# Optimization experiments

Measured on AMD Instinct MI355X. Metric: run time of the kernel, lower is better.

Reference implementation:

```python
import jax, jax.numpy as jnp
import numpy as np

N = 40000        # total gene nodes
E = 640000       # edges
F_IN = 128       # num_features
H = 128          # hidden_dim
SUB = 400        # genes per cell
EPS = 1e-5


def _bn(x, g, b):
    # BatchNorm1d, training-mode batch statistics (biased variance), deterministic
    m = x.mean(axis=0)
    v = x.var(axis=0)
    return (x - m) * jax.lax.rsqrt(v + EPS) * g + b


def _gcn_conv(x, W, b, src, dst):
    # PyG GCNConv: h = X W; add self-loops; symmetric deg^{-1/2} normalization;
    # scatter-add messages from src into dst; then add bias.
    h = x @ W                                   # [N, H]
    loop = jnp.arange(N)
    s = jnp.concatenate([src, loop])            # [E+N]
    d = jnp.concatenate([dst, loop])
    deg = jax.ops.segment_sum(jnp.ones(s.shape[0], h.dtype), d, num_segments=N)
    dis = jnp.where(deg > 0, deg ** -0.5, 0.0)  # deg_inv_sqrt
    norm = dis[s] * dis[d]                      # [E+N]
    out = jax.ops.segment_sum(h[s] * norm[:, None], d, num_segments=N)
    return out + b


def setup_inputs() -> dict:
    key = jax.random.key(0)
    ks = jax.random.split(key, 16)
    sc = lambda fan: 1.0 / np.sqrt(fan)
    inp = {
        "x": jax.random.normal(ks[0], (N, F_IN), jnp.float32),
        "edge_index": jax.random.randint(ks[1], (2, E), 0, N, jnp.int64),
        "conv1_w": jax.random.normal(ks[2], (F_IN, H), jnp.float32) * sc(F_IN),
        "conv1_b": jnp.zeros((H,), jnp.float32),
        "bn1_g": jnp.ones((H,), jnp.float32),
        "bn1_b": jnp.zeros((H,), jnp.float32),
        "conv2_w": jax.random.normal(ks[3], (H, H), jnp.float32) * sc(H),
        "conv2_b": jnp.zeros((H,), jnp.float32),
        "bn2_g": jnp.ones((H,), jnp.float32),
        "bn2_b": jnp.zeros((H,), jnp.float32),
        "att_w1": jax.random.normal(ks[4], (H, H // 2), jnp.float32) * sc(H),
        "att_b1": jnp.zeros((H // 2,), jnp.float32),
        "att_w2": jax.random.normal(ks[5], (H // 2, 1), jnp.float32) * sc(H // 2),
        "att_b2": jnp.zeros((1,), jnp.float32),
        "fc_w": jax.random.normal(ks[6], (H, H), jnp.float32) * sc(H),
        "fc_b": jnp.zeros((H,), jnp.float32),
        "bne_g": jnp.ones((H,), jnp.float32),
        "bne_b": jnp.zeros((H,), jnp.float32),
        "bot_w": jax.random.normal(ks[7], (H, 32), jnp.float32) * sc(H),
        "bot_b": jnp.zeros((32,), jnp.float32),
        "bnb_g": jnp.ones((32,), jnp.float32),
        "bnb_b": jnp.zeros((32,), jnp.float32),
    }
    return inp


def reference(x, edge_index, conv1_w, conv1_b, bn1_g, bn1_b,
              conv2_w, conv2_b, bn2_g, bn2_b,
              att_w1, att_b1, att_w2, att_b2,
              fc_w, fc_b, bne_g, bne_b,
              bot_w, bot_b, bnb_g, bnb_b):
    src, dst = edge_index[0], edge_index[1]
    # embed: two GCNConv + BN + ReLU (dropout omitted: deterministic reference)
    h = jax.nn.relu(_bn(_gcn_conv(x, conv1_w, conv1_b, src, dst), bn1_g, bn1_b))
    emb = jax.nn.relu(_bn(_gcn_conv(h, conv2_w, conv2_b, src, dst), bn2_g, bn2_b))
    # attention pooling over genes within each cell
    num_cells = N // SUB
    xr = emb.reshape(num_cells, SUB, H)                      # [C, S, H]
    scores = jnp.tanh(xr @ att_w1 + att_b1) @ att_w2 + att_b2  # [C, S, 1]
    w = jax.nn.softmax(scores, axis=1)
    pooled = jnp.sum(xr * w, axis=1)                          # [C, H]
    # dense head
    y = jax.nn.relu(_bn(pooled @ fc_w + fc_b, bne_g, bne_b))
    y = jax.nn.relu(_bn(y @ bot_w + bot_b, bnb_g, bnb_b))     # [C, 32]
    return (y, emb)
```

## Files before the change

kernel.cpp:

```cpp
#include <hip/hip_runtime.h>
#include <math.h>

typedef unsigned int u32;
typedef __attribute__((ext_vector_type(8))) short bf16x8;
typedef __attribute__((ext_vector_type(4))) float f32x4;

#define NN   40000
#define EE   640000
#define SUBG 400
#define CELLS 100
#define BNEPS 1e-5f
#define GB   2048
#define GEMMB 625
#define FILLB 1024

__device__ __forceinline__ u32 bf16pair(float a, float b) {
    u32 ua = __float_as_uint(a), ub = __float_as_uint(b);
    ua += 0x7fffu + ((ua >> 16) & 1u);
    ub += 0x7fffu + ((ub >> 16) & 1u);
    return (ua >> 16) | (ub & 0xffff0000u);
}
__device__ __forceinline__ float bflo(u32 u) { return __uint_as_float(u << 16); }
__device__ __forceinline__ float bfhi(u32 u) { return __uint_as_float(u & 0xffff0000u); }

#define SWZ(g, cc) ( ((cc) & 3) | (((((cc) >> 2) ^ ((g) & 15))) << 2) )

__global__ void k_init(int* deg_cursor, const float* W1, u32* Wt1,
                       const float* W2, u32* Wt2, const float* wa, u32* Wta,
                       float* hstats) {
    int i = blockIdx.x * 256 + threadIdx.x;
    if (i < 2 * NN) { deg_cursor[i] = 0; return; }
    i -= 2 * NN;
    if (i < 16384) {
        const float* W = (i < 8192) ? W1 : W2;
        u32* Wt = (i < 8192) ? Wt1 : Wt2;
        int j = i & 8191;
        int n = j >> 6, k2 = (j & 63) * 2;
        Wt[n * 64 + (j & 63)] = bf16pair(W[k2 * 128 + n], W[(k2 + 1) * 128 + n]);
        return;
    }
    i -= 16384;
    if (i < 4096) {
        int n = i >> 6, k2 = (i & 63) * 2;
        Wta[n * 64 + (i & 63)] = bf16pair(wa[k2 * 64 + n], wa[(k2 + 1) * 64 + n]);
        return;
    }
    i -= 4096;
    if (i < 320) hstats[i] = 0.f;
}

__global__ void k_degcount(const int* __restrict__ dst, int* __restrict__ deg) {
    int i = blockIdx.x * blockDim.x + threadIdx.x;
    int stride = gridDim.x * blockDim.x;
    for (; i < EE; i += stride) atomicAdd(&deg[dst[i]], 1);
}

__global__ __launch_bounds__(1024)
void k_scan(const int* __restrict__ deg, int* __restrict__ rowstart,
            float* __restrict__ dis) {
    __shared__ int ps[1024];
    int t = threadIdx.x;
    const int4* d4 = (const int4*)deg;
    int sum = 0;
#pragma unroll
    for (int j = 0; j < 10; ++j) {
        int i4 = t * 10 + j;
        if (i4 < 10000) {
            int4 v = d4[i4];
            sum += v.x + v.y + v.z + v.w;
        }
    }
    ps[t] = sum;
    __syncthreads();
    for (int off = 1; off < 1024; off <<= 1) {
        int add = (t >= off) ? ps[t - off] : 0;
        __syncthreads();
        ps[t] += add;
        __syncthreads();
    }
    int run = ps[t] - sum;
#pragma unroll
    for (int j = 0; j < 10; ++j) {
        int i4 = t * 10 + j;
        if (i4 < 10000) {
            int4 v = d4[i4];
            int4 r;
            r.x = run;
            r.y = run + v.x;
            r.z = r.y + v.y;
            r.w = r.z + v.z;
            run = r.w + v.w;
            *(int4*)&rowstart[i4 * 4] = r;
            float4 dv;
            dv.x = rsqrtf((float)(v.x + 1));
            dv.y = rsqrtf((float)(v.y + 1));
            dv.z = rsqrtf((float)(v.z + 1));
            dv.w = rsqrtf((float)(v.w + 1));
            *(float4*)&dis[i4 * 4] = dv;
        }
    }
    if (t == 0) rowstart[NN] = EE;
}

__global__ __launch_bounds__(256)
void k_fillgemm(const float* __restrict__ X, const u32* __restrict__ Wt,
                u32* __restrict__ Yb, const float* __restrict__ dis,
                const int* __restrict__ src, const int* __restrict__ dst,
                const int* __restrict__ rowstart, int* __restrict__ cursor,
                int* __restrict__ csr_src) {
    int bid = blockIdx.x;
    int t = threadIdx.x;
    if (bid >= GEMMB) {
        int i = (bid - GEMMB) * 256 + t;
        int stride = FILLB * 256;
        for (; i < EE; i += stride) {
            int d = dst[i];
            int slot = rowstart[d] + atomicAdd(&cursor[d], 1);
            csr_src[slot] = src[i];
        }
        return;
    }
    int l = t & 63, wv = t >> 6;
    int rowbase = bid * 64 + wv * 16;
    int ml = l & 15, kg = l >> 4;

    f32x4 acc[8];
#pragma unroll
    for (int nt = 0; nt < 8; ++nt) acc[nt] = (f32x4){0.f, 0.f, 0.f, 0.f};
    const float* xr = X + (long)(rowbase + ml) * 128;
#pragma unroll
    for (int kk = 0; kk < 4; ++kk) {
        int k0 = kk * 32 + kg * 8;
        float4 xa = *(const float4*)&xr[k0];
        float4 xb = *(const float4*)&xr[k0 + 4];
        union { u32 u[4]; bf16x8 v; } af;
        af.u[0] = bf16pair(xa.x, xa.y);
        af.u[1] = bf16pair(xa.z, xa.w);
        af.u[2] = bf16pair(xb.x, xb.y);
        af.u[3] = bf16pair(xb.z, xb.w);
#pragma unroll
        for (int nt = 0; nt < 8; ++nt) {
            bf16x8 b = *(const bf16x8*)&Wt[(nt * 16 + ml) * 64 + (k0 >> 1)];
            acc[nt] = __builtin_amdgcn_mfma_f32_16x16x32_bf16(af.v, b, acc[nt], 0, 0, 0);
        }
    }
#pragma unroll
    for (int r = 0; r < 4; ++r) {
        int m = rowbase + kg * 4 + r;
        float dd = dis[m];
        long obase = (long)m * 64;
#pragma unroll
        for (int nt = 0; nt < 8; ++nt) {
            float v = acc[nt][r] * dd;
            float v2 = __shfl_xor(v, 1);
            if ((l & 1) == 0)
                Yb[obase + nt * 8 + (ml >> 1)] = bf16pair(v, v2);
        }
    }
}

__global__ __launch_bounds__(256)
void k_gemm_bf16(const u32* __restrict__ Xb, const u32* __restrict__ Wt,
                 u32* __restrict__ Yb, const float* __restrict__ ss,
                 const float* __restrict__ dis) {
    int t = threadIdx.x;
    int l = t & 63, wv = t >> 6;
    int rowbase = blockIdx.x * 64 + wv * 16;
    int ml = l & 15, kg = l >> 4;

    f32x4 acc[8];
#pragma unroll
    for (int nt = 0; nt < 8; ++nt) acc[nt] = (f32x4){0.f, 0.f, 0.f, 0.f};
    const u32* xr = Xb + (long)(rowbase + ml) * 64;
#pragma unroll
    for (int kk = 0; kk < 4; ++kk) {
        int k0 = kk * 32 + kg * 8;
        uint4 xw = *(const uint4*)&xr[k0 >> 1];
        float f0 = bflo(xw.x), f1 = bfhi(xw.x), f2 = bflo(xw.y), f3 = bfhi(xw.y);
        float f4 = bflo(xw.z), f5 = bfhi(xw.z), f6 = bflo(xw.w), f7 = bfhi(xw.w);
        float4 sca = *(const float4*)&ss[k0];
        float4 sha = *(const float4*)&ss[128 + k0];
        float4 scb = *(const float4*)&ss[k0 + 4];
        float4 shb = *(const float4*)&ss[128 + k0 + 4];
        f0 = fmaxf(fmaf(f0, sca.x, sha.x), 0.f);
        f1 = fmaxf(fmaf(f1, sca.y, sha.y), 0.f);
        f2 = fmaxf(fmaf(f2, sca.z, sha.z), 0.f);
        f3 = fmaxf(fmaf(f3, sca.w, sha.w), 0.f);
        f4 = fmaxf(fmaf(f4, scb.x, shb.x), 0.f);
        f5 = fmaxf(fmaf(f5, scb.y, shb.y), 0.f);
        f6 = fmaxf(fmaf(f6, scb.z, shb.z), 0.f);
        f7 = fmaxf(fmaf(f7, scb.w, shb.w), 0.f);
        union { u32 u[4]; bf16x8 v; } af;
        af.u[0] = bf16pair(f0, f1);
        af.u[1] = bf16pair(f2, f3);
        af.u[2] = bf16pair(f4, f5);
        af.u[3] = bf16pair(f6, f7);
#pragma unroll
        for (int nt = 0; nt < 8; ++nt) {
            bf16x8 b = *(const bf16x8*)&Wt[(nt * 16 + ml) * 64 + (k0 >> 1)];
            acc[nt] = __builtin_amdgcn_mfma_f32_16x16x32_bf16(af.v, b, acc[nt], 0, 0, 0);
        }
    }
#pragma unroll
    for (int r = 0; r < 4; ++r) {
        int m = rowbase + kg * 4 + r;
        float dd = dis[m];
        long obase = (long)m * 64;
#pragma unroll
        for (int nt = 0; nt < 8; ++nt) {
            float v = acc[nt][r] * dd;
            float v2 = __shfl_xor(v, 1);
            if ((l & 1) == 0)
                Yb[obase + nt * 8 + (ml >> 1)] = bf16pair(v, v2);
        }
    }
}

__global__ __launch_bounds__(256)
void k_gather_stats(const uint4* __restrict__ Hb, const int* __restrict__ rowstart,
                    const int* __restrict__ csr_src, const float* __restrict__ dis,
                    const float* __restrict__ bias, u32* __restrict__ F1b,
                    float* __restrict__ part) {
    __shared__ float ls[1024], lq[1024];
    int t = threadIdx.x;
    int lane = t & 63, wv = t >> 6;
    int gw = blockIdx.x * 4 + wv;
    int g = lane >> 4, p = lane & 15;
    int c0 = p * 8 + g * 2;
    float2 bb = *(const float2*)&bias[c0];
    float s0 = 0.f, s1 = 0.f, q0 = 0.f, q1 = 0.f;

    for (int node = gw; node < NN; node += GB * 4) {
        float a0 = 0.f, a1 = 0.f, a2 = 0.f, a3 = 0.f, a4 = 0.f, a5 = 0.f, a6 = 0.f, a7 = 0.f;
        if (g == 0) {
            uint4 h = Hb[node * 16 + p];
            a0 = bflo(h.x); a1 = bfhi(h.x);
            a2 = bflo(h.y); a3 = bfhi(h.y);
            a4 = bflo(h.z); a5 = bfhi(h.z);
            a6 = bflo(h.w); a7 = bfhi(h.w);
        }
        int e1 = rowstart[node + 1];
        int e = rowstart[node] + g;
        for (; e + 4 < e1; e += 8) {
            int sA = csr_src[e];
            int sB = csr_src[e + 4];
            uint4 h0 = Hb[sA * 16 + p];
            uint4 h1 = Hb[sB * 16 + p];
            a0 += bflo(h0.x); a1 += bfhi(h0.x);
            a2 += bflo(h0.y); a3 += bfhi(h0.y);
            a4 += bflo(h0.z); a5 += bfhi(h0.z);
            a6 += bflo(h0.w); a7 += bfhi(h0.w);
            a0 += bflo(h1.x); a1 += bfhi(h1.x);
            a2 += bflo(h1.y); a3 += bfhi(h1.y);
            a4 += bflo(h1.z); a5 += bfhi(h1.z);
            a6 += bflo(h1.w); a7 += bfhi(h1.w);
        }
        if (e < e1) {
            int sA = csr_src[e];
            uint4 h0 = Hb[sA * 16 + p];
            a0 += bflo(h0.x); a1 += bfhi(h0.x);
            a2 += bflo(h0.y); a3 += bfhi(h0.y);
            a4 += bflo(h0.z); a5 += bfhi(h0.z);
            a6 += bflo(h0.w); a7 += bfhi(h0.w);
        }
#pragma unroll
        for (int m = 16; m <= 32; m <<= 1) {
            a0 += __shfl_xor(a0, m); a1 += __shfl_xor(a1, m);
            a2 += __shfl_xor(a2, m); a3 += __shfl_xor(a3, m);
            a4 += __shfl_xor(a4, m); a5 += __shfl_xor(a5, m);
            a6 += __shfl_xor(a6, m); a7 += __shfl_xor(a7, m);
        }
        float dd = dis[node];
        float x = (g == 0) ? a0 : (g == 1) ? a2 : (g == 2) ? a4 : a6;
        float y = (g == 0) ? a1 : (g == 1) ? a3 : (g == 2) ? a5 : a7;
        x = fmaf(x, dd, bb.x);
        y = fmaf(y, dd, bb.y);
        u32 pw = bf16pair(x, y);
        F1b[node * 64 + (c0 >> 1)] = pw;
        float rx = bflo(pw), ry = bfhi(pw);
        s0 += rx; s1 += ry; q0 += rx * rx; q1 += ry * ry;
    }
    ls[wv * 128 + c0] = s0; ls[wv * 128 + c0 + 1] = s1;
    lq[wv * 128 + c0] = q0; lq[wv * 128 + c0 + 1] = q1;
    __syncthreads();
    if (t < 128) {
        float S = ls[t] + ls[128 + t] + ls[256 + t] + ls[384 + t];
        float Q = lq[t] + lq[128 + t] + lq[256 + t] + lq[384 + t];
        part[blockIdx.x * 256 + t] = S;
        part[blockIdx.x * 256 + 128 + t] = Q;
    }
}

__global__ __launch_bounds__(256)
void k_bnfinalw(const float* __restrict__ part, const float* __restrict__ g,
                const float* __restrict__ b, float* __restrict__ ss) {
    __shared__ float rs[256], rq[256];
    int c = blockIdx.x, t = threadIdx.x;
    float s = 0.f, q = 0.f;
    for (int i = t; i < GB; i += 256) {
        s += part[i * 256 + c];
        q += part[i * 256 + 128 + c];
    }
    rs[t] = s; rq[t] = q;
    __syncthreads();
    for (int off = 128; off > 0; off >>= 1) {
        if (t < off) { rs[t] += rs[t + off]; rq[t] += rq[t + off]; }
        __syncthreads();
    }
    if (t == 0) {
        float mean = rs[0] * (1.0f / NN);
        float var  = rq[0] * (1.0f / NN) - mean * mean;
        float sc = g[c] * rsqrtf(var + BNEPS);
        ss[c] = sc;
        ss[128 + c] = b[c] - mean * sc;
    }
}

__global__ __launch_bounds__(512, 1)
void k_cell(const u32* __restrict__ F1b, const float* __restrict__ ss,
            float* __restrict__ emb,
            const u32* __restrict__ Wta, const float* __restrict__ b1,
            const float* __restrict__ w2, const float* __restrict__ b2,
            const float* __restrict__ fc_w, const float* __restrict__ fc_b,
            float* __restrict__ y1pre, float* __restrict__ hstats) {
    __shared__ u32 xs[SUBG * 64];
    __shared__ float sc[SUBG];
    __shared__ float red[512];
    __shared__ float pr[128];
    int c = blockIdx.x;
    int t = threadIdx.x;
    long gbase = (long)c * SUBG;

    for (int i = t; i < SUBG * 64; i += 512) {
        int gg = i >> 6, cc = i & 63;
        u32 v = F1b[(gbase + gg) * 64 + cc];
        float x0 = bflo(v), x1 = bfhi(v);
        float2 scv = *(const float2*)&ss[2 * cc];
        float2 shv = *(const float2*)&ss[128 + 2 * cc];
        x0 = fmaxf(fmaf(x0, scv.x, shv.x), 0.f);
        x1 = fmaxf(fmaf(x1, scv.y, shv.y), 0.f);
        float2 o = { x0, x1 };
        *(float2*)&emb[(gbase + gg) * 128 + 2 * cc] = o;
        xs[gg * 64 + SWZ(gg, cc)] = bf16pair(x0, x1);
    }
    __syncthreads();

    int l = t & 63, wv = t >> 6;
    int ml = l & 15, kg = l >> 4;
    bf16x8 bw[4][4];
#pragma unroll
    for (int nt = 0; nt < 4; ++nt)
#pragma unroll
        for (int kk = 0; kk < 4; ++kk)
            bw[nt][kk] = *(const bf16x8*)&Wta[(nt * 16 + ml) * 64 + (kk * 16 + kg * 4)];
    float b1v[4], w2v[4];
#pragma unroll
    for (int nt = 0; nt < 4; ++nt) {
        b1v[nt] = b1[nt * 16 + ml];
        w2v[nt] = w2[nt * 16 + ml];
    }
    float b2v = b2[0];

    for (int tile = wv; tile < 25; tile += 8) {
        int gg = tile * 16 + ml;
        f32x4 acc[4];
#pragma unroll
        for (int nt = 0; nt < 4; ++nt) acc[nt] = (f32x4){0.f, 0.f, 0.f, 0.f};
#pragma unroll
        for (int kk = 0; kk < 4; ++kk) {
            int cc4 = kk * 4 + kg;
            bf16x8 a = *(const bf16x8*)&xs[gg * 64 + ((cc4 ^ ml) << 2)];
#pragma unroll
            for (int nt = 0; nt < 4; ++nt)
                acc[nt] = __builtin_amdgcn_mfma_f32_16x16x32_bf16(a, bw[nt][kk], acc[nt], 0, 0, 0);
        }
#pragma unroll
        for (int r = 0; r < 4; ++r) {
            int g2 = tile * 16 + kg * 4 + r;
            float s = tanhf(acc[0][r] + b1v[0]) * w2v[0]
                    + tanhf(acc[1][r] + b1v[1]) * w2v[1]
                    + tanhf(acc[2][r] + b1v[2]) * w2v[2]
                    + tanhf(acc[3][r] + b1v[3]) * w2v[3];
            s += __shfl_xor(s, 1);
            s += __shfl_xor(s, 2);
            s += __shfl_xor(s, 4);
            s += __shfl_xor(s, 8);
            if (ml == 0) sc[g2] = s + b2v;
        }
    }
    __syncthreads();

    red[t] = (t < SUBG) ? sc[t] : -1e30f;
    __syncthreads();
    for (int off = 256; off > 0; off >>= 1) {
        if (t < off) red[t] = fmaxf(red[t], red[t + off]);
        __syncthreads();
    }
    float mx = red[0];
    __syncthreads();
    float e = 0.f;
    if (t < SUBG) { e = __expf(sc[t] - mx); }
    red[t] = e;
    __syncthreads();
    for (int off = 256; off > 0; off >>= 1) {
        if (t < off) red[t] += red[t + off];
        __syncthreads();
    }
    float inv = 1.0f / red[0];
    __syncthreads();
    if (t < SUBG) sc[t] = e * inv;
    __syncthreads();

    int col = t & 127, grp = t >> 7;
    int cc = col >> 1, lohi = col & 1;
    float acc = 0.f;
    for (int gg = grp; gg < SUBG; gg += 4) {
        u32 v = xs[gg * 64 + SWZ(gg, cc)];
        float val = lohi ? bfhi(v) : bflo(v);
        acc += sc[gg] * val;
    }
    red[t] = acc;
    __syncthreads();
    if (t < 128) pr[col] = red[col] + red[128 + col] + red[256 + col] + red[384 + col];
    __syncthreads();

    if (t < 128) {
        float a1 = fc_b[t];
#pragma unroll 4
        for (int k = 0; k < 128; ++k) a1 = fmaf(pr[k], fc_w[k * 128 + t], a1);
        y1pre[c * 128 + t] = a1;
        atomicAdd(&hstats[t], a1);
        atomicAdd(&hstats[128 + t], a1 * a1);
    }
}

__global__ __launch_bounds__(128)
void k_head2s(const float* __restrict__ y1pre, const float* __restrict__ hstats,
              const float* __restrict__ bne_g, const float* __restrict__ bne_b,
              const float* __restrict__ bot_w, const float* __restrict__ bot_b,
              float* __restrict__ y2pre, float* __restrict__ hstats2) {
    __shared__ float row[128];
    int c = blockIdx.x, t = threadIdx.x;
    float s = hstats[t], q = hstats[128 + t];
    float mean = s * 0.01f, var = q * 0.01f - mean * mean;
    float scv = bne_g[t] * rsqrtf(var + BNEPS);
    float shv = bne_b[t] - mean * scv;
    row[t] = fmaxf(fmaf(y1pre[c * 128 + t], scv, shv), 0.f);
    __syncthreads();
    if (t < 32) {
        float a2 = bot_b[t];
#pragma unroll 4
        for (int k = 0; k < 128; ++k) a2 = fmaf(row[k], bot_w[k * 32 + t], a2);
        y2pre[c * 32 + t] = a2;
        atomicAdd(&hstats2[t], a2);
        atomicAdd(&hstats2[32 + t], a2 * a2);
    }
}

__global__ __launch_bounds__(256)
void k_out(const float* __restrict__ y2pre, const float* __restrict__ hstats2,
           const float* __restrict__ bnb_g, const float* __restrict__ bnb_b,
           float* __restrict__ y_out) {
    __shared__ float scv[32], shv[32];
    int t = threadIdx.x;
    if (t < 32) {
        float s = hstats2[t], q = hstats2[32 + t];
        float mean = s * 0.01f, var = q * 0.01f - mean * mean;
        float v = bnb_g[t] * rsqrtf(var + BNEPS);
        scv[t] = v; shv[t] = bnb_b[t] - mean * v;
    }
    __syncthreads();
    for (int i = t; i < CELLS * 32; i += 256)
        y_out[i] = fmaxf(fmaf(y2pre[i], scv[i & 31], shv[i & 31]), 0.f);
}

extern "C" void kernel_launch(void* const* d_in, const int* in_sizes, int n_in,
                              void* d_out, int out_size, void* d_ws, size_t ws_size,
                              hipStream_t stream) {
    const float* x        = (const float*)d_in[0];
    const int*   ei       = (const int*)d_in[1];
    const float* conv1_w  = (const float*)d_in[2];
    const float* conv1_b  = (const float*)d_in[3];
    const float* bn1_g    = (const float*)d_in[4];
    const float* bn1_b    = (const float*)d_in[5];
    const float* conv2_w  = (const float*)d_in[6];
    const float* conv2_b  = (const float*)d_in[7];
    const float* bn2_g    = (const float*)d_in[8];
    const float* bn2_b    = (const float*)d_in[9];
    const float* att_w1   = (const float*)d_in[10];
    const float* att_b1   = (const float*)d_in[11];
    const float* att_w2   = (const float*)d_in[12];
    const float* att_b2   = (const float*)d_in[13];
    const float* fc_w     = (const float*)d_in[14];
    const float* fc_b     = (const float*)d_in[15];
    const float* bne_g    = (const float*)d_in[16];
    const float* bne_b    = (const float*)d_in[17];
    const float* bot_w    = (const float*)d_in[18];
    const float* bot_b    = (const float*)d_in[19];
    const float* bnb_g    = (const float*)d_in[20];
    const float* bnb_b    = (const float*)d_in[21];

    const int* src = ei;
    const int* dst = ei + EE;

    float* y_out   = (float*)d_out;
    float* emb_out = y_out + CELLS * 32;

    float* ws = (float*)d_ws;
    u32*   Hb     = (u32*)ws;
    u32*   F1b    = Hb + (long)NN * 64;
    float* dis    = (float*)(F1b + (long)NN * 64);
    float* part   = dis + NN;
    float* ss     = part + GB * 256;
    float* hstats = ss + 256;
    float* y1pre  = hstats + 320;
    float* y2pre  = y1pre + CELLS * 128;
    u32*   Wt1    = (u32*)(y2pre + CELLS * 32);
    u32*   Wt2    = Wt1 + 8192;
    u32*   Wta    = Wt2 + 8192;
    int*   deg    = (int*)(Wta + 4096);
    int*   cursor = deg + NN;
    int*   rowstart = cursor + NN;
    int*   csr_src  = rowstart + NN + 1;

    k_init<<<394, 256, 0, stream>>>(deg, conv1_w, Wt1, conv2_w, Wt2, att_w1, Wta, hstats);
    k_degcount<<<512, 256, 0, stream>>>(dst, deg);
    k_scan<<<1, 1024, 0, stream>>>(deg, rowstart, dis);
    k_fillgemm<<<GEMMB + FILLB, 256, 0, stream>>>(x, Wt1, Hb, dis, src, dst,
                                                  rowstart, cursor, csr_src);
    k_gather_stats<<<GB, 256, 0, stream>>>((const uint4*)Hb, rowstart, csr_src, dis,
                                           conv1_b, F1b, part);
    k_bnfinalw<<<128, 256, 0, stream>>>(part, bn1_g, bn1_b, ss);
    k_gemm_bf16<<<GEMMB, 256, 0, stream>>>(F1b, Wt2, Hb, ss, dis);
    k_gather_stats<<<GB, 256, 0, stream>>>((const uint4*)Hb, rowstart, csr_src, dis,
                                           conv2_b, F1b, part);
    k_bnfinalw<<<128, 256, 0, stream>>>(part, bn2_g, bn2_b, ss);
    k_cell<<<CELLS, 512, 0, stream>>>(F1b, ss, emb_out, Wta, att_b1, att_w2, att_b2,
                                      fc_w, fc_b, y1pre, hstats);
    k_head2s<<<CELLS, 128, 0, stream>>>(y1pre, hstats, bne_g, bne_b, bot_w, bot_b,
                                        y2pre, hstats + 256);
    k_out<<<1, 256, 0, stream>>>(y2pre, hstats + 256, bnb_g, bnb_b, y_out);
}
```

Baseline: 244.4 us.

## Split per-cell attention kernel across many blocks and move first GEMM earlier

```diff
diff --git a/kernel.cpp b/kernel.cpp
--- a/kernel.cpp
+++ b/kernel.cpp
@@ -10,9 +10,11 @@
 #define SUBG 400
 #define CELLS 100
 #define BNEPS 1e-5f
-#define GB   2048
+#define GB    2048
 #define GEMMB 625
+#define DEGB  512
 #define FILLB 1024
+#define SCALEB 2500
 
 __device__ __forceinline__ u32 bf16pair(float a, float b) {
     u32 ua = __float_as_uint(a), ub = __float_as_uint(b);
@@ -22,8 +24,6 @@
 }
 __device__ __forceinline__ float bflo(u32 u) { return __uint_as_float(u << 16); }
 __device__ __forceinline__ float bfhi(u32 u) { return __uint_as_float(u & 0xffff0000u); }
-
-#define SWZ(g, cc) ( ((cc) & 3) | (((((cc) >> 2) ^ ((g) & 15))) << 2) )
 
 __global__ void k_init(int* deg_cursor, const float* W1, u32* Wt1,
                        const float* W2, u32* Wt2, const float* wa, u32* Wta,
@@ -49,10 +49,54 @@
     if (i < 320) hstats[i] = 0.f;
 }
 
-__global__ void k_degcount(const int* __restrict__ dst, int* __restrict__ deg) {
-    int i = blockIdx.x * blockDim.x + threadIdx.x;
-    int stride = gridDim.x * blockDim.x;
-    for (; i < EE; i += stride) atomicAdd(&deg[dst[i]], 1);
+__global__ __launch_bounds__(256)
+void k_gemmdeg(const float* __restrict__ X, const u32* __restrict__ Wt,
+               u32* __restrict__ Yb, const int* __restrict__ dst,
+               int* __restrict__ deg) {
+    int bid = blockIdx.x;
+    int t = threadIdx.x;
+    if (bid >= GEMMB) {
+        int i = (bid - GEMMB) * 256 + t;
+        int stride = DEGB * 256;
+        for (; i < EE; i += stride) atomicAdd(&deg[dst[i]], 1);
+        return;
+    }
+    int l = t & 63, wv = t >> 6;
+    int rowbase = bid * 64 + wv * 16;
+    int ml = l & 15, kg = l >> 4;
+
+    f32x4 acc[8];
+#pragma unroll
+    for (int nt = 0; nt < 8; ++nt) acc[nt] = (f32x4){0.f, 0.f, 0.f, 0.f};
+    const float* xr = X + (long)(rowbase + ml) * 128;
+#pragma unroll
+    for (int kk = 0; kk < 4; ++kk) {
+        int k0 = kk * 32 + kg * 8;
+        float4 xa = *(const float4*)&xr[k0];
+        float4 xb = *(const float4*)&xr[k0 + 4];
+        union { u32 u[4]; bf16x8 v; } af;
+        af.u[0] = bf16pair(xa.x, xa.y);
+        af.u[1] = bf16pair(xa.z, xa.w);
+        af.u[2] = bf16pair(xb.x, xb.y);
+        af.u[3] = bf16pair(xb.z, xb.w);
+#pragma unroll
+        for (int nt = 0; nt < 8; ++nt) {
+            bf16x8 b = *(const bf16x8*)&Wt[(nt * 16 + ml) * 64 + (k0 >> 1)];
+            acc[nt] = __builtin_amdgcn_mfma_f32_16x16x32_bf16(af.v, b, acc[nt], 0, 0, 0);
+        }
+    }
+#pragma unroll
+    for (int r = 0; r < 4; ++r) {
+        int m = rowbase + kg * 4 + r;
+        long obase = (long)m * 64;
+#pragma unroll
+        for (int nt = 0; nt < 8; ++nt) {
+            float v = acc[nt][r];
+            float v2 = __shfl_xor(v, 1);
+            if ((l & 1) == 0)
+                Yb[obase + nt * 8 + (ml >> 1)] = bf16pair(v, v2);
+        }
+    }
 }
 
 __global__ __launch_bounds__(1024)
@@ -103,15 +147,14 @@
 }
 
 __global__ __launch_bounds__(256)
-void k_fillgemm(const float* __restrict__ X, const u32* __restrict__ Wt,
-                u32* __restrict__ Yb, const float* __restrict__ dis,
-                const int* __restrict__ src, const int* __restrict__ dst,
-                const int* __restrict__ rowstart, int* __restrict__ cursor,
-                int* __restrict__ csr_src) {
+void k_fillscale(const int* __restrict__ src, const int* __restrict__ dst,
+                 const int* __restrict__ rowstart, int* __restrict__ cursor,
+                 int* __restrict__ csr_src, uint4* __restrict__ Hb,
+                 const float* __restrict__ dis) {
     int bid = blockIdx.x;
     int t = threadIdx.x;
-    if (bid >= GEMMB) {
-        int i = (bid - GEMMB) * 256 + t;
+    if (bid < FILLB) {
+        int i = bid * 256 + t;
         int stride = FILLB * 256;
         for (; i < EE; i += stride) {
             int d = dst[i];
@@ -120,43 +163,14 @@
         }
         return;
     }
-    int l = t & 63, wv = t >> 6;
-    int rowbase = bid * 64 + wv * 16;
-    int ml = l & 15, kg = l >> 4;
-
-    f32x4 acc[8];
-#pragma unroll
-    for (int nt = 0; nt < 8; ++nt) acc[nt] = (f32x4){0.f, 0.f, 0.f, 0.f};
-    const float* xr = X + (long)(rowbase + ml) * 128;
-#pragma unroll
-    for (int kk = 0; kk < 4; ++kk) {
-        int k0 = kk * 32 + kg * 8;
-        float4 xa = *(const float4*)&xr[k0];
-        float4 xb = *(const float4*)&xr[k0 + 4];
-        union { u32 u[4]; bf16x8 v; } af;
-        af.u[0] = bf16pair(xa.x, xa.y);
-        af.u[1] = bf16pair(xa.z, xa.w);
-        af.u[2] = bf16pair(xb.x, xb.y);
-        af.u[3] = bf16pair(xb.z, xb.w);
-#pragma unroll
-        for (int nt = 0; nt < 8; ++nt) {
-            bf16x8 b = *(const bf16x8*)&Wt[(nt * 16 + ml) * 64 + (k0 >> 1)];
-            acc[nt] = __builtin_amdgcn_mfma_f32_16x16x32_bf16(af.v, b, acc[nt], 0, 0, 0);
-        }
-    }
-#pragma unroll
-    for (int r = 0; r < 4; ++r) {
-        int m = rowbase + kg * 4 + r;
-        float dd = dis[m];
-        long obase = (long)m * 64;
-#pragma unroll
-        for (int nt = 0; nt < 8; ++nt) {
-            float v = acc[nt][r] * dd;
-            float v2 = __shfl_xor(v, 1);
-            if ((l & 1) == 0)
-                Yb[obase + nt * 8 + (ml >> 1)] = bf16pair(v, v2);
-        }
-    }
+    int i = (bid - FILLB) * 256 + t;
+    float dd = dis[i >> 4];
+    uint4 v = Hb[i];
+    v.x = bf16pair(bflo(v.x) * dd, bfhi(v.x) * dd);
+    v.y = bf16pair(bflo(v.y) * dd, bfhi(v.y) * dd);
+    v.z = bf16pair(bflo(v.z) * dd, bfhi(v.z) * dd);
+    v.w = bf16pair(bflo(v.w) * dd, bfhi(v.w) * dd);
+    Hb[i] = v;
 }
 
 __global__ __launch_bounds__(256)
@@ -316,43 +330,55 @@
     }
 }
 
-__global__ __launch_bounds__(512, 1)
-void k_cell(const u32* __restrict__ F1b, const float* __restrict__ ss,
-            float* __restrict__ emb,
-            const u32* __restrict__ Wta, const float* __restrict__ b1,
-            const float* __restrict__ w2, const float* __restrict__ b2,
-            const float* __restrict__ fc_w, const float* __restrict__ fc_b,
-            float* __restrict__ y1pre, float* __restrict__ hstats) {
-    __shared__ u32 xs[SUBG * 64];
-    __shared__ float sc[SUBG];
-    __shared__ float red[512];
-    __shared__ float pr[128];
-    int c = blockIdx.x;
-    int t = threadIdx.x;
-    long gbase = (long)c * SUBG;
-
-    for (int i = t; i < SUBG * 64; i += 512) {
-        int gg = i >> 6, cc = i & 63;
-        u32 v = F1b[(gbase + gg) * 64 + cc];
-        float x0 = bflo(v), x1 = bfhi(v);
-        float2 scv = *(const float2*)&ss[2 * cc];
-        float2 shv = *(const float2*)&ss[128 + 2 * cc];
-        x0 = fmaxf(fmaf(x0, scv.x, shv.x), 0.f);
-        x1 = fmaxf(fmaf(x1, scv.y, shv.y), 0.f);
-        float2 o = { x0, x1 };
-        *(float2*)&emb[(gbase + gg) * 128 + 2 * cc] = o;
-        xs[gg * 64 + SWZ(gg, cc)] = bf16pair(x0, x1);
-    }
-    __syncthreads();
-
+__global__ __launch_bounds__(256)
+void k_scoremb(const u32* __restrict__ F1b, const float* __restrict__ ss,
+               float* __restrict__ emb,
+               const u32* __restrict__ Wta, const float* __restrict__ b1,
+               const float* __restrict__ w2, const float* __restrict__ b2,
+               float* __restrict__ scores) {
+    int t = threadIdx.x;
     int l = t & 63, wv = t >> 6;
+    int rowbase = blockIdx.x * 64 + wv * 16;
     int ml = l & 15, kg = l >> 4;
-    bf16x8 bw[4][4];
-#pragma unroll
-    for (int nt = 0; nt < 4; ++nt)
-#pragma unroll
-        for (int kk = 0; kk < 4; ++kk)
-            bw[nt][kk] = *(const bf16x8*)&Wta[(nt * 16 + ml) * 64 + (kk * 16 + kg * 4)];
+
+    f32x4 acc[4];
+#pragma unroll
+    for (int nt = 0; nt < 4; ++nt) acc[nt] = (f32x4){0.f, 0.f, 0.f, 0.f};
+    const u32* xr = F1b + (long)(rowbase + ml) * 64;
+    float* er = emb + (long)(rowbase + ml) * 128;
+#pragma unroll
+    for (int kk = 0; kk < 4; ++kk) {
+        int k0 = kk * 32 + kg * 8;
+        uint4 xw = *(const uint4*)&xr[k0 >> 1];
+        float f0 = bflo(xw.x), f1 = bfhi(xw.x), f2 = bflo(xw.y), f3 = bfhi(xw.y);
+        float f4 = bflo(xw.z), f5 = bfhi(xw.z), f6 = bflo(xw.w), f7 = bfhi(xw.w);
+        float4 sca = *(const float4*)&ss[k0];
+        float4 sha = *(const float4*)&ss[128 + k0];
+        float4 scb = *(const float4*)&ss[k0 + 4];
+        float4 shb = *(const float4*)&ss[128 + k0 + 4];
+        f0 = fmaxf(fmaf(f0, sca.x, sha.x), 0.f);
+        f1 = fmaxf(fmaf(f1, sca.y, sha.y), 0.f);
+        f2 = fmaxf(fmaf(f2, sca.z, sha.z), 0.f);
+        f3 = fmaxf(fmaf(f3, sca.w, sha.w), 0.f);
+        f4 = fmaxf(fmaf(f4, scb.x, shb.x), 0.f);
+        f5 = fmaxf(fmaf(f5, scb.y, shb.y), 0.f);
+        f6 = fmaxf(fmaf(f6, scb.z, shb.z), 0.f);
+        f7 = fmaxf(fmaf(f7, scb.w, shb.w), 0.f);
+        float4 e0 = { f0, f1, f2, f3 };
+        float4 e1 = { f4, f5, f6, f7 };
+        *(float4*)&er[k0] = e0;
+        *(float4*)&er[k0 + 4] = e1;
+        union { u32 u[4]; bf16x8 v; } af;
+        af.u[0] = bf16pair(f0, f1);
+        af.u[1] = bf16pair(f2, f3);
+        af.u[2] = bf16pair(f4, f5);
+        af.u[3] = bf16pair(f6, f7);
+#pragma unroll
+        for (int nt = 0; nt < 4; ++nt) {
+            bf16x8 b = *(const bf16x8*)&Wta[(nt * 16 + ml) * 64 + (k0 >> 1)];
+            acc[nt] = __builtin_amdgcn_mfma_f32_16x16x32_bf16(af.v, b, acc[nt], 0, 0, 0);
+        }
+    }
     float b1v[4], w2v[4];
 #pragma unroll
     for (int nt = 0; nt < 4; ++nt) {
@@ -360,78 +386,97 @@
         w2v[nt] = w2[nt * 16 + ml];
     }
     float b2v = b2[0];
-
-    for (int tile = wv; tile < 25; tile += 8) {
-        int gg = tile * 16 + ml;
-        f32x4 acc[4];
-#pragma unroll
-        for (int nt = 0; nt < 4; ++nt) acc[nt] = (f32x4){0.f, 0.f, 0.f, 0.f};
-#pragma unroll
-        for (int kk = 0; kk < 4; ++kk) {
-            int cc4 = kk * 4 + kg;
-            bf16x8 a = *(const bf16x8*)&xs[gg * 64 + ((cc4 ^ ml) << 2)];
-#pragma unroll
-            for (int nt = 0; nt < 4; ++nt)
-                acc[nt] = __builtin_amdgcn_mfma_f32_16x16x32_bf16(a, bw[nt][kk], acc[nt], 0, 0, 0);
-        }
-#pragma unroll
-        for (int r = 0; r < 4; ++r) {
-            int g2 = tile * 16 + kg * 4 + r;
-            float s = tanhf(acc[0][r] + b1v[0]) * w2v[0]
-                    + tanhf(acc[1][r] + b1v[1]) * w2v[1]
-                    + tanhf(acc[2][r] + b1v[2]) * w2v[2]
-                    + tanhf(acc[3][r] + b1v[3]) * w2v[3];
-            s += __shfl_xor(s, 1);
-            s += __shfl_xor(s, 2);
-            s += __shfl_xor(s, 4);
-            s += __shfl_xor(s, 8);
-            if (ml == 0) sc[g2] = s + b2v;
-        }
-    }
-    __syncthreads();
-
-    red[t] = (t < SUBG) ? sc[t] : -1e30f;
-    __syncthreads();
-    for (int off = 256; off > 0; off >>= 1) {
+#pragma unroll
+    for (int r = 0; r < 4; ++r) {
+        float s = tanhf(acc[0][r] + b1v[0]) * w2v[0]
+                + tanhf(acc[1][r] + b1v[1]) * w2v[1]
+                + tanhf(acc[2][r] + b1v[2]) * w2v[2]
+                + tanhf(acc[3][r] + b1v[3]) * w2v[3];
+        s += __shfl_xor(s, 1);
+        s += __shfl_xor(s, 2);
+        s += __shfl_xor(s, 4);
+        s += __shfl_xor(s, 8);
+        if (ml == 0) scores[rowbase + kg * 4 + r] = s + b2v;
+    }
+}
+
+__global__ __launch_bounds__(256)
+void k_pool4(const u32* __restrict__ F1b, const float* __restrict__ ss,
+             const float* __restrict__ scores, float* __restrict__ pp) {
+    __shared__ float sl[SUBG];
+    __shared__ float red[256];
+    __shared__ float rbuf[512];
+    int b = blockIdx.x;
+    int c = b >> 2, q = b & 3;
+    int t = threadIdx.x;
+    int base = c * SUBG;
+
+    float lmax = -1e30f;
+    for (int i = t; i < SUBG; i += 256) {
+        float v = scores[base + i];
+        sl[i] = v;
+        lmax = fmaxf(lmax, v);
+    }
+    red[t] = lmax;
+    __syncthreads();
+    for (int off = 128; off > 0; off >>= 1) {
         if (t < off) red[t] = fmaxf(red[t], red[t + off]);
         __syncthreads();
     }
     float mx = red[0];
     __syncthreads();
-    float e = 0.f;
-    if (t < SUBG) { e = __expf(sc[t] - mx); }
-    red[t] = e;
-    __syncthreads();
-    for (int off = 256; off > 0; off >>= 1) {
+    float lsum = 0.f;
+    for (int i = t; i < SUBG; i += 256) {
+        float e = __expf(sl[i] - mx);
+        sl[i] = e;
+        lsum += e;
+    }
+    red[t] = lsum;
+    __syncthreads();
+    for (int off = 128; off > 0; off >>= 1) {
         if (t < off) red[t] += red[t + off];
         __syncthreads();
     }
     float inv = 1.0f / red[0];
     __syncthreads();
-    if (t < SUBG) sc[t] = e * inv;
-    __syncthreads();
-
-    int col = t & 127, grp = t >> 7;
-    int cc = col >> 1, lohi = col & 1;
-    float acc = 0.f;
-    for (int gg = grp; gg < SUBG; gg += 4) {
-        u32 v = xs[gg * 64 + SWZ(gg, cc)];
-        float val = lohi ? bfhi(v) : bflo(v);
-        acc += sc[gg] * val;
-    }
-    red[t] = acc;
-    __syncthreads();
-    if (t < 128) pr[col] = red[col] + red[128 + col] + red[256 + col] + red[384 + col];
-    __syncthreads();
-
-    if (t < 128) {
-        float a1 = fc_b[t];
+
+    int cc = t & 63, gp = t >> 6;
+    float2 scv = *(const float2*)&ss[2 * cc];
+    float2 shv = *(const float2*)&ss[128 + 2 * cc];
+    int g0 = q * 100 + gp * 25;
+    float a0 = 0.f, a1 = 0.f;
+#pragma unroll 5
+    for (int j = 0; j < 25; ++j) {
+        int gg = g0 + j;
+        u32 v = F1b[(long)(base + gg) * 64 + cc];
+        float w = sl[gg] * inv;
+        float x0 = fmaxf(fmaf(bflo(v), scv.x, shv.x), 0.f);
+        float x1 = fmaxf(fmaf(bfhi(v), scv.y, shv.y), 0.f);
+        a0 += w * x0;
+        a1 += w * x1;
+    }
+    rbuf[gp * 128 + 2 * cc] = a0;
+    rbuf[gp * 128 + 2 * cc + 1] = a1;
+    __syncthreads();
+    if (t < 128)
+        pp[b * 128 + t] = rbuf[t] + rbuf[128 + t] + rbuf[256 + t] + rbuf[384 + t];
+}
+
+__global__ __launch_bounds__(128)
+void k_head1r(const float* __restrict__ pp, const float* __restrict__ fc_w,
+              const float* __restrict__ fc_b, float* __restrict__ y1pre,
+              float* __restrict__ hstats) {
+    __shared__ float pr[128];
+    int c = blockIdx.x, t = threadIdx.x;
+    pr[t] = pp[(c * 4 + 0) * 128 + t] + pp[(c * 4 + 1) * 128 + t]
+          + pp[(c * 4 + 2) * 128 + t] + pp[(c * 4 + 3) * 128 + t];
+    __syncthreads();
+    float a1 = fc_b[t];
 #pragma unroll 4
-        for (int k = 0; k < 128; ++k) a1 = fmaf(pr[k], fc_w[k * 128 + t], a1);
-        y1pre[c * 128 + t] = a1;
-        atomicAdd(&hstats[t], a1);
-        atomicAdd(&hstats[128 + t], a1 * a1);
-    }
+    for (int k = 0; k < 128; ++k) a1 = fmaf(pr[k], fc_w[k * 128 + t], a1);
+    y1pre[c * 128 + t] = a1;
+    atomicAdd(&hstats[t], a1);
+    atomicAdd(&hstats[128 + t], a1 * a1);
 }
 
 __global__ __launch_bounds__(128)
@@ -515,7 +560,9 @@
     float* hstats = ss + 256;
     float* y1pre  = hstats + 320;
     float* y2pre  = y1pre + CELLS * 128;
-    u32*   Wt1    = (u32*)(y2pre + CELLS * 32);
+    float* scores = y2pre + CELLS * 32;
+    float* pp     = scores + NN;
+    u32*   Wt1    = (u32*)(pp + 400 * 128);
     u32*   Wt2    = Wt1 + 8192;
     u32*   Wta    = Wt2 + 8192;
     int*   deg    = (int*)(Wta + 4096);
@@ -524,10 +571,10 @@
     int*   csr_src  = rowstart + NN + 1;
 
     k_init<<<394, 256, 0, stream>>>(deg, conv1_w, Wt1, conv2_w, Wt2, att_w1, Wta, hstats);
-    k_degcount<<<512, 256, 0, stream>>>(dst, deg);
+    k_gemmdeg<<<GEMMB + DEGB, 256, 0, stream>>>(x, Wt1, Hb, dst, deg);
     k_scan<<<1, 1024, 0, stream>>>(deg, rowstart, dis);
-    k_fillgemm<<<GEMMB + FILLB, 256, 0, stream>>>(x, Wt1, Hb, dis, src, dst,
-                                                  rowstart, cursor, csr_src);
+    k_fillscale<<<FILLB + SCALEB, 256, 0, stream>>>(src, dst, rowstart, cursor,
+                                                    csr_src, (uint4*)Hb, dis);
     k_gather_stats<<<GB, 256, 0, stream>>>((const uint4*)Hb, rowstart, csr_src, dis,
                                            conv1_b, F1b, part);
     k_bnfinalw<<<128, 256, 0, stream>>>(part, bn1_g, bn1_b, ss);
@@ -535,8 +582,10 @@
     k_gather_stats<<<GB, 256, 0, stream>>>((const uint4*)Hb, rowstart, csr_src, dis,
                                            conv2_b, F1b, part);
     k_bnfinalw<<<128, 256, 0, stream>>>(part, bn2_g, bn2_b, ss);
-    k_cell<<<CELLS, 512, 0, stream>>>(F1b, ss, emb_out, Wta, att_b1, att_w2, att_b2,
-                                      fc_w, fc_b, y1pre, hstats);
+    k_scoremb<<<GEMMB, 256, 0, stream>>>(F1b, ss, emb_out, Wta, att_b1, att_w2,
+                                         att_b2, scores);
+    k_pool4<<<4 * CELLS, 256, 0, stream>>>(F1b, ss, scores, pp);
+    k_head1r<<<CELLS, 128, 0, stream>>>(pp, fc_w, fc_b, y1pre, hstats);
     k_head2s<<<CELLS, 128, 0, stream>>>(y1pre, hstats, bne_g, bne_b, bot_w, bot_b,
                                         y2pre, hstats + 256);
     k_out<<<1, 256, 0, stream>>>(y2pre, hstats + 256, bnb_g, bnb_b, y_out);
```

After: 235.6 us (median of 2 runs). 1.04x faster.
